# Optimization experiments

Measured on AMD Instinct MI355X. Metric: run time of the kernel, lower is better.

Reference implementation:

```python
import jax, jax.numpy as jnp
import numpy as np

ROUTES = 1152
CAPS = 10
IN_CH = 8
OUT_CH = 16
BATCH = 256
NUM_ITER = 3


def setup_inputs() -> dict:
    key = jax.random.key(0)
    kx, kw = jax.random.split(key)
    x = jax.random.normal(kx, (BATCH, ROUTES, IN_CH), dtype=jnp.float32)
    # W corresponds to nn.Parameter of shape [1, routes, caps, out, in]; leading 1 dropped.
    W = jax.random.normal(kw, (ROUTES, CAPS, OUT_CH, IN_CH), dtype=jnp.float32)
    return {"x": x, "W": W}


def _squash(s):
    # Faithful to source: sum of squares over the trailing singleton dim -> elementwise.
    sq = s * s
    return sq * s / ((1.0 + sq) * jnp.sqrt(sq))


def reference(x, W):
    # u_hat[b,r,c,o] = W[r,c,o,i] @ x[b,r,i]
    u_hat = jnp.einsum("rcoi,bri->brco", W, x)
    b_ij = jnp.zeros((ROUTES, CAPS), dtype=x.dtype)
    v = None
    for it in range(NUM_ITER):
        # legacy F.softmax on 4D [1,R,C,1] tensor -> softmax over dim=1 (routes)
        c_ij = jax.nn.softmax(b_ij, axis=0)  # [R, C]
        s_j = jnp.einsum("rc,brco->bco", c_ij, u_hat)  # [B, C, O]
        v = _squash(s_j)
        if it < NUM_ITER - 1:
            # a_ij[b,r,c] = <u_hat[b,r,c,:], v[b,c,:]>; b_ij += mean over batch
            a_ij = jnp.einsum("brco,bco->brc", u_hat, v)
            b_ij = b_ij + a_ij.mean(axis=0)
    # original returns v_j.squeeze(1) with shape [B, caps, out, 1]
    return v[..., None]
```

## Files before the change

### kernel.cpp

```cpp
#include <hip/hip_runtime.h>
#include <math.h>

namespace {

constexpr int B_ = 256;
constexpr int R_ = 1152;
constexpr int C_ = 10;
constexpr int O_ = 16;
constexpr int I_ = 8;
constexpr int CO_ = C_ * O_;
constexpr int WRI_ = C_ * O_ * I_;

constexpr int KS_  = 32;
constexpr int RC_  = R_ / KS_;

constexpr int NBA_   = 512;
constexpr int NBA2_  = 384;

constexpr int KSF_ = 16;
constexpr int RCF_ = R_ / KSF_;
constexpr int MBF_ = 16;

constexpr size_t XT_OFF    = 0;
constexpr size_t XT_N      = (size_t)R_ * B_ * I_;
constexpr size_t SA_OFF    = XT_OFF + XT_N;
constexpr size_t SAB_N     = (size_t)CO_ * B_;
constexpr size_t SB_OFF    = SA_OFF + SAB_N;
constexpr size_t BIJ_OFF   = SB_OFF + SAB_N;
constexpr size_t BIJ_N     = (size_t)C_ * R_;
constexpr size_t ZERO_N    = 2 * SAB_N + BIJ_N;
constexpr size_t FL_TOTAL  = BIJ_OFF + BIJ_N;

__device__ __forceinline__ float rcp_fast(float x) {
#if defined(__has_builtin)
#if __has_builtin(__builtin_amdgcn_rcpf)
    return __builtin_amdgcn_rcpf(x);
#else
    return 1.0f / x;
#endif
#else
    return 1.0f / x;
#endif
}

__device__ __forceinline__ float squashf(float s) {
    return s * fabsf(s) / (1.0f + s * s);
}

__device__ __forceinline__ float squash_fast(float s) {
    return s * fabsf(s) * rcp_fast(1.0f + s * s);
}

__global__ __launch_bounds__(256) void k_tr(const float* __restrict__ x,
                                            float* __restrict__ xT,
                                            float* __restrict__ zbase) {
    __shared__ float t[8][32][8];
    const int tid = threadIdx.x;
    {
        const int gi = blockIdx.x * 256 + tid;
        if (gi < (int)(ZERO_N / 4))
            ((float4*)zbase)[gi] = make_float4(0.f, 0.f, 0.f, 0.f);
    }
    const int r0 = (blockIdx.x % 36) * 32;
    const int b0 = (blockIdx.x / 36) * 8;
    {
        const int rl = tid & 31, bl = tid >> 5;
        const float4* p = (const float4*)(x + ((size_t)(b0 + bl) * R_ + (r0 + rl)) * I_);
        const float4 a0 = p[0], a1 = p[1];
        float* d = &t[bl][rl][0];
        *(float4*)d = a0;
        *(float4*)(d + 4) = a1;
    }
    __syncthreads();
    {
        const int f = tid & 7, rw = tid >> 3;
        const float* s8 = &t[f][rw][0];
        const float4 a0 = *(const float4*)s8, a1 = *(const float4*)(s8 + 4);
        float* d = xT + ((size_t)(r0 + rw) * B_ + (b0 + f)) * I_;
        *(float4*)d = a0;
        *(float4*)(d + 4) = a1;
    }
}

template <bool UNIFORM>
__global__ __launch_bounds__(256) void k_s8(const float* __restrict__ xT,
                                            const float* __restrict__ Wm,
                                            const float* __restrict__ bijT,
                                            float* __restrict__ s_dst) {
    __shared__ __align__(16) float wl[RC_ * 128];
    __shared__ float cwch[RC_];
    __shared__ float sred[8];

    const int tid   = threadIdx.x;
    const int lane  = tid & 63;
    const int bid   = blockIdx.x;
    const int c     = bid >> 6;
    const int chunk = bid & 63;
    const int ks    = chunk >> 1;
    const int bh    = chunk & 1;
    const int r0    = ks * RC_;

    if (!UNIFORM) {
        const float* bc = bijT + (size_t)c * R_;
        float bv[5];
        float m = -1e30f;
        #pragma unroll
        for (int k = 0; k < 5; ++k) {
            const int r = tid + 256 * k;
            bv[k] = (r < R_) ? bc[r] : -1e30f;
            m = fmaxf(m, bv[k]);
        }
        #pragma unroll
        for (int off = 32; off > 0; off >>= 1)
            m = fmaxf(m, __shfl_down(m, off, 64));
        if (lane == 0) sred[tid >> 6] = m;
        __syncthreads();
        const float bm = fmaxf(fmaxf(sred[0], sred[1]), fmaxf(sred[2], sred[3]));
        float se = 0.f;
        #pragma unroll
        for (int k = 0; k < 5; ++k)
            se += (bv[k] > -1e29f) ? expf(bv[k] - bm) : 0.f;
        #pragma unroll
        for (int off = 32; off > 0; off >>= 1)
            se += __shfl_down(se, off, 64);
        if (lane == 0) sred[4 + (tid >> 6)] = se;
        __syncthreads();
        const float inv = 1.0f / (sred[4] + sred[5] + sred[6] + sred[7]);
        if (tid < RC_) cwch[tid] = expf(bc[r0 + tid] - bm) * inv;
        __syncthreads();
    }

    {
        const float4* src = (const float4*)(Wm + ((size_t)r0 * C_ + c) * 128);
        float4* dst = (float4*)wl;
        #pragma unroll
        for (int k = 0; k < (RC_ * 32 + 255) / 256; ++k) {
            const int idx = tid + 256 * k;
            if (idx < RC_ * 32) {
                const int r = idx >> 5, q = idx & 31;
                float4 wv = src[(size_t)r * (C_ * 32) + q];
                const float cw = UNIFORM ? (1.0f / (float)R_) : cwch[r];
                wv.x *= cw; wv.y *= cw; wv.z *= cw; wv.w *= cw;
                dst[idx] = wv;
            }
        }
    }
    __syncthreads();

    const int o0 = (tid >> 6) * 4;
    const float* xbase = xT + ((size_t)r0 * B_ + bh * 128 + lane) * I_;

    float acc[4][2];
    #pragma unroll
    for (int oo = 0; oo < 4; ++oo) { acc[oo][0] = 0.f; acc[oo][1] = 0.f; }

    #pragma unroll 2
    for (int r = 0; r < RC_; ++r) {
        const float* xr = xbase + (size_t)r * B_ * I_;
        const float4 a00 = ((const float4*)xr)[0];
        const float4 a01 = ((const float4*)xr)[1];
        const float4 a10 = ((const float4*)(xr + 64 * I_))[0];
        const float4 a11 = ((const float4*)(xr + 64 * I_))[1];
        const float4* wp = (const float4*)&wl[r * 128 + o0 * 8];
        #pragma unroll
        for (int oo = 0; oo < 4; ++oo) {
            const float4 w0 = wp[oo * 2 + 0];
            const float4 w1 = wp[oo * 2 + 1];
            float a = acc[oo][0];
            a = fmaf(a00.x, w0.x, a);
            a = fmaf(a00.y, w0.y, a);
            a = fmaf(a00.z, w0.z, a);
            a = fmaf(a00.w, w0.w, a);
            a = fmaf(a01.x, w1.x, a);
            a = fmaf(a01.y, w1.y, a);
            a = fmaf(a01.z, w1.z, a);
            a = fmaf(a01.w, w1.w, a);
            acc[oo][0] = a;
            float b = acc[oo][1];
            b = fmaf(a10.x, w0.x, b);
            b = fmaf(a10.y, w0.y, b);
            b = fmaf(a10.z, w0.z, b);
            b = fmaf(a10.w, w0.w, b);
            b = fmaf(a11.x, w1.x, b);
            b = fmaf(a11.y, w1.y, b);
            b = fmaf(a11.z, w1.z, b);
            b = fmaf(a11.w, w1.w, b);
            acc[oo][1] = b;
        }
    }

    float* sp = s_dst + (size_t)(c * O_ + o0) * B_ + bh * 128 + lane;
    #pragma unroll
    for (int oo = 0; oo < 4; ++oo) {
        atomicAdd(sp + (size_t)oo * B_, acc[oo][0]);
        atomicAdd(sp + (size_t)oo * B_ + 64, acc[oo][1]);
    }
}

struct A8Sh {
    float4 xsw[3 * 512];
    float  part[3][320];
};

template <int NR>
__device__ __forceinline__ void a8_body(int r0, A8Sh& sh,
                                        const float* __restrict__ xT,
                                        const float* __restrict__ Wm,
                                        const float* __restrict__ s_read,
                                        float* __restrict__ bij_dst) {
    const int tid = threadIdx.x;

    {
        const float4* src = (const float4*)(xT + (size_t)r0 * B_ * I_);
        for (int k = tid; k < NR * 512; k += 320)
            sh.xsw[k ^ ((k >> 6) & 7)] = src[k];
    }
    __syncthreads();

    const int cq = tid % 40;
    const int bg = tid / 40;
    const int b0 = bg * 32;

    float acc[NR][4][8];
    #pragma unroll
    for (int rr = 0; rr < NR; ++rr)
        #pragma unroll
        for (int j = 0; j < 4; ++j)
            #pragma unroll
            for (int i = 0; i < 8; ++i) acc[rr][j][i] = 0.f;

    const float* vbase = s_read + (size_t)(4 * cq) * B_ + b0;

    #pragma unroll 2
    for (int bb = 0; bb < 32; bb += 4) {
        float va[4][4];
        #pragma unroll
        for (int j = 0; j < 4; ++j) {
            const float4 t = *(const float4*)(vbase + (size_t)j * B_ + bb);
            va[j][0] = squash_fast(t.x);
            va[j][1] = squash_fast(t.y);
            va[j][2] = squash_fast(t.z);
            va[j][3] = squash_fast(t.w);
        }
        #pragma unroll
        for (int j2 = 0; j2 < 4; ++j2) {
            const int eb = (b0 + bb + j2) * 2;
            #pragma unroll
            for (int rr = 0; rr < NR; ++rr) {
                const float4 x0 = sh.xsw[(rr * 512 + eb) ^ bg];
                const float4 x1 = sh.xsw[(rr * 512 + eb + 1) ^ bg];
                #pragma unroll
                for (int j = 0; j < 4; ++j) {
                    const float w = va[j][j2];
                    acc[rr][j][0] = fmaf(w, x0.x, acc[rr][j][0]);
                    acc[rr][j][1] = fmaf(w, x0.y, acc[rr][j][1]);
                    acc[rr][j][2] = fmaf(w, x0.z, acc[rr][j][2]);
                    acc[rr][j][3] = fmaf(w, x0.w, acc[rr][j][3]);
                    acc[rr][j][4] = fmaf(w, x1.x, acc[rr][j][4]);
                    acc[rr][j][5] = fmaf(w, x1.y, acc[rr][j][5]);
                    acc[rr][j][6] = fmaf(w, x1.z, acc[rr][j][6]);
                    acc[rr][j][7] = fmaf(w, x1.w, acc[rr][j][7]);
                }
            }
        }
    }

    #pragma unroll
    for (int rr = 0; rr < NR; ++rr) {
        const float* wp = Wm + (((size_t)(r0 + rr)) * CO_ + 4 * cq) * I_;
        float psum = 0.f;
        #pragma unroll
        for (int j = 0; j < 4; ++j) {
            const float4 w0 = *(const float4*)(wp + j * 8);
            const float4 w1 = *(const float4*)(wp + j * 8 + 4);
            float p = acc[rr][j][0] * w0.x;
            p = fmaf(acc[rr][j][1], w0.y, p);
            p = fmaf(acc[rr][j][2], w0.z, p);
            p = fmaf(acc[rr][j][3], w0.w, p);
            p = fmaf(acc[rr][j][4], w1.x, p);
            p = fmaf(acc[rr][j][5], w1.y, p);
            p = fmaf(acc[rr][j][6], w1.z, p);
            p = fmaf(acc[rr][j][7], w1.w, p);
            psum += p;
        }
        sh.part[rr][tid] = psum;
    }
    __syncthreads();

    if (tid < NR * C_) {
        const int r = tid / C_, c2 = tid % C_;
        float s = 0.f;
        #pragma unroll
        for (int g2 = 0; g2 < 8; ++g2)
            #pragma unroll
            for (int q = 0; q < 4; ++q)
                s += sh.part[r][g2 * 40 + c2 * 4 + q];
        bij_dst[(size_t)c2 * R_ + (r0 + r)] += s * (1.0f / (float)B_);
    }
}

__global__ __launch_bounds__(320) void k_a8(const float* __restrict__ xT,
                                            const float* __restrict__ Wm,
                                            const float* __restrict__ s_read,
                                            float* __restrict__ s_zero,
                                            float* __restrict__ bijT) {
    __shared__ A8Sh sh;
    const int bid = blockIdx.x;
    if (s_zero != nullptr && bid < 40 && threadIdx.x < 256) {
        ((float4*)s_zero)[bid * 256 + threadIdx.x] =
            make_float4(0.f, 0.f, 0.f, 0.f);
    }
    if (bid < NBA2_) {
        a8_body<2>(bid * 2, sh, xT, Wm, s_read, bijT);
    } else {
        a8_body<3>(NBA2_ * 2 + (bid - NBA2_) * 3, sh, xT, Wm, s_read, bijT);
    }
}

__global__ __launch_bounds__(256) void k_sqout(const float* __restrict__ s,
                                               float* __restrict__ out) {
    const int co = blockIdx.x;
    const int b  = threadIdx.x;
    out[(size_t)b * CO_ + co] = squash_fast(s[(size_t)co * B_ + b]);
}

template <bool UNIFORM>
__global__ __launch_bounds__(256) void k_s_f(const float* __restrict__ x,
                                             const float* __restrict__ Wm,
                                             const float* __restrict__ cij,
                                             float* __restrict__ s_out) {
    const int o  = threadIdx.x & 15;
    const int tb = threadIdx.x >> 4;
    const int b  = blockIdx.z * MBF_ + tb;
    const int c  = blockIdx.y;
    const int r0 = blockIdx.x * RCF_;

    const float* xp = x + ((size_t)b * R_ + r0) * I_;
    const float* wp = Wm + (((size_t)r0 * C_ + c) * O_ + o) * I_;
    const float* cp = cij + (size_t)r0 * C_ + c;

    float acc = 0.f;
    #pragma unroll 4
    for (int r = 0; r < RCF_; ++r) {
        const float4 xv0 = *(const float4*)(xp);
        const float4 xv1 = *(const float4*)(xp + 4);
        const float4 wv0 = *(const float4*)(wp);
        const float4 wv1 = *(const float4*)(wp + 4);
        const float p0 = fmaf(xv0.y, wv0.y, xv0.x * wv0.x);
        const float p1 = fmaf(xv0.w, wv0.w, xv0.z * wv0.z);
        const float p2 = fmaf(xv1.y, wv1.y, xv1.x * wv1.x);
        const float p3 = fmaf(xv1.w, wv1.w, xv1.z * wv1.z);
        const float cw = UNIFORM ? (1.0f / (float)R_) : cp[0];
        acc = fmaf(cw, (p0 + p1) + (p2 + p3), acc);
        xp += I_;
        wp += WRI_;
        cp += C_;
    }
    atomicAdd(&s_out[((size_t)b * C_ + c) * O_ + o], acc);
}

__global__ __launch_bounds__(256) void k_a_f(const float* __restrict__ x,
                                             const float* __restrict__ Wm,
                                             const float* __restrict__ s_in,
                                             float* __restrict__ amean) {
    __shared__ __align__(16) float wlds[2 * WRI_];
    __shared__ float red[4][2 * C_];

    const int tid = threadIdx.x;
    const int r0  = blockIdx.x * 2;

    const float* wsrc = Wm + (size_t)r0 * WRI_;
    #pragma unroll
    for (int k = 0; k < 2 * WRI_ / 256; ++k)
        wlds[tid + 256 * k] = wsrc[tid + 256 * k];
    __syncthreads();

    const int b    = tid;
    const int lane = tid & 63;
    const int wv   = tid >> 6;

    float xv[2][I_];
    const float4* xp4 = (const float4*)(x + ((size_t)b * R_ + r0) * I_);
    #pragma unroll
    for (int rr = 0; rr < 2; ++rr) {
        const float4 a0 = xp4[rr * 2 + 0];
        const float4 a1 = xp4[rr * 2 + 1];
        xv[rr][0] = a0.x; xv[rr][1] = a0.y; xv[rr][2] = a0.z; xv[rr][3] = a0.w;
        xv[rr][4] = a1.x; xv[rr][5] = a1.y; xv[rr][6] = a1.z; xv[rr][7] = a1.w;
    }

    #pragma unroll 1
    for (int c = 0; c < C_; ++c) {
        const float4* sp4 = (const float4*)(s_in + ((size_t)b * C_ + c) * O_);
        float v[O_];
        #pragma unroll
        for (int q = 0; q < 4; ++q) {
            const float4 sv = sp4[q];
            v[q * 4 + 0] = squashf(sv.x);
            v[q * 4 + 1] = squashf(sv.y);
            v[q * 4 + 2] = squashf(sv.z);
            v[q * 4 + 3] = squashf(sv.w);
        }
        #pragma unroll 1
        for (int rr = 0; rr < 2; ++rr) {
            const float4* wl4 = (const float4*)&wlds[(rr * C_ + c) * O_ * I_];
            float a = 0.f;
            #pragma unroll
            for (int o = 0; o < O_; ++o) {
                const float4 w0 = wl4[o * 2 + 0];
                const float4 w1 = wl4[o * 2 + 1];
                float u = xv[rr][0] * w0.x;
                u = fmaf(xv[rr][1], w0.y, u);
                u = fmaf(xv[rr][2], w0.z, u);
                u = fmaf(xv[rr][3], w0.w, u);
                u = fmaf(xv[rr][4], w1.x, u);
                u = fmaf(xv[rr][5], w1.y, u);
                u = fmaf(xv[rr][6], w1.z, u);
                u = fmaf(xv[rr][7], w1.w, u);
                a = fmaf(u, v[o], a);
            }
            #pragma unroll
            for (int off = 32; off > 0; off >>= 1)
                a += __shfl_down(a, off, 64);
            if (lane == 0) red[wv][rr * C_ + c] = a;
        }
    }

    __syncthreads();
    if (tid < 2 * C_) {
        const float t = red[0][tid] + red[1][tid] + red[2][tid] + red[3][tid];
        const int rr = tid / C_;
        const int c  = tid % C_;
        amean[(size_t)(r0 + rr) * C_ + c] = t * (1.0f / (float)B_);
    }
}

__global__ __launch_bounds__(256) void k_soft(const float* __restrict__ amean,
                                              float* __restrict__ bij,
                                              float* __restrict__ cij) {
    const int c   = blockIdx.x;
    const int tid = threadIdx.x;
    __shared__ float sred[4];

    float vals[5];
    float m = -1e30f;
    #pragma unroll
    for (int k = 0; k < 5; ++k) {
        const int r = tid + 256 * k;
        if (r < R_) {
            const size_t idx = (size_t)r * C_ + c;
            const float vv = bij[idx] + amean[idx];
            bij[idx] = vv;
            vals[k] = vv;
            m = fmaxf(m, vv);
        } else {
            vals[k] = -1e30f;
        }
    }
    #pragma unroll
    for (int off = 32; off > 0; off >>= 1)
        m = fmaxf(m, __shfl_down(m, off, 64));
    if ((tid & 63) == 0) sred[tid >> 6] = m;
    __syncthreads();
    const float bm = fmaxf(fmaxf(sred[0], sred[1]), fmaxf(sred[2], sred[3]));
    __syncthreads();

    float se = 0.f;
    #pragma unroll
    for (int k = 0; k < 5; ++k)
        se += (vals[k] > -1e29f) ? expf(vals[k] - bm) : 0.f;
    #pragma unroll
    for (int off = 32; off > 0; off >>= 1)
        se += __shfl_down(se, off, 64);
    if ((tid & 63) == 0) sred[tid >> 6] = se;
    __syncthreads();
    const float inv = 1.0f / (sred[0] + sred[1] + sred[2] + sred[3]);

    #pragma unroll
    for (int k = 0; k < 5; ++k) {
        const int r = tid + 256 * k;
        if (r < R_) cij[(size_t)r * C_ + c] = expf(vals[k] - bm) * inv;
    }
}

__global__ __launch_bounds__(256) void k_squash(float* __restrict__ s) {
    const int idx = blockIdx.x * 256 + threadIdx.x;
    if (idx < B_ * CO_) s[idx] = squashf(s[idx]);
}

}

extern "C" void kernel_launch(void* const* d_in, const int* in_sizes, int n_in,
                              void* d_out, int out_size, void* d_ws, size_t ws_size,
                              hipStream_t stream) {
    const float* x  = (const float*)d_in[0];
    const float* Wm = (const float*)d_in[1];
    float* out = (float*)d_out;
    float* ws  = (float*)d_ws;

    const size_t need = FL_TOTAL * sizeof(float);

    if (ws_size >= need) {
        float* xT   = ws + XT_OFF;
        float* sA   = ws + SA_OFF;
        float* sB   = ws + SB_OFF;
        float* bijT = ws + BIJ_OFF;

        k_tr<<<1152, 256, 0, stream>>>(x, xT, sA );

        k_s8<true><<<C_ * 64, 256, 0, stream>>>(xT, Wm, bijT, sA);
        k_a8<<<NBA_, 320, 0, stream>>>(xT, Wm, sA, nullptr, bijT);

        k_s8<false><<<C_ * 64, 256, 0, stream>>>(xT, Wm, bijT, sB);
        k_a8<<<NBA_, 320, 0, stream>>>(xT, Wm, sB, sA , bijT);

        k_s8<false><<<C_ * 64, 256, 0, stream>>>(xT, Wm, bijT, sA);
        k_sqout<<<CO_, 256, 0, stream>>>(sA, out);
    } else {
        float* s_buf = ws;
        float* cij   = ws + 40960;
        float* bij   = cij + R_ * C_;
        float* amean = bij + R_ * C_;

        const dim3 gsf(KSF_, C_, B_ / MBF_);

        hipMemsetAsync(bij, 0, R_ * C_ * sizeof(float), stream);

        hipMemsetAsync(s_buf, 0, B_ * CO_ * sizeof(float), stream);
        k_s_f<true><<<gsf, 256, 0, stream>>>(x, Wm, cij, s_buf);
        k_a_f<<<R_ / 2, 256, 0, stream>>>(x, Wm, s_buf, amean);
        k_soft<<<C_, 256, 0, stream>>>(amean, bij, cij);

        hipMemsetAsync(s_buf, 0, B_ * CO_ * sizeof(float), stream);
        k_s_f<false><<<gsf, 256, 0, stream>>>(x, Wm, cij, s_buf);
        k_a_f<<<R_ / 2, 256, 0, stream>>>(x, Wm, s_buf, amean);
        k_soft<<<C_, 256, 0, stream>>>(amean, bij, cij);

        hipMemsetAsync(out, 0, B_ * CO_ * sizeof(float), stream);
        k_s_f<false><<<gsf, 256, 0, stream>>>(x, Wm, cij, out);
        k_squash<<<(B_ * CO_ + 255) / 256, 256, 0, stream>>>(out);
    }
}
```

Baseline: 195.4 us.

## Split routing kernels across batch halves and double route-chunk count

The s-kernel now splits routes into 64 chunks instead of 32, doubling its grid. The agreement kernel is replaced by k_a9, which handles two routes per block for only half the batch, so there are twice as many blocks, each with less shared memory. Per-route b_ij updates now combine the two batch halves with atomicAdd instead of a plain accumulate. The aim is more parallelism and occupancy on the many-CU GPU, at the cost of more atomics on s and b_ij and smaller per-block work.

Result: slower. 202.0 us (+3.4%).

```diff
diff --git a/kernel.cpp b/kernel.cpp
--- a/kernel.cpp
+++ b/kernel.cpp
@@ -11,11 +11,11 @@
 constexpr int CO_ = C_ * O_;
 constexpr int WRI_ = C_ * O_ * I_;
 
-constexpr int KS_  = 32;
+constexpr int KS_  = 64;
 constexpr int RC_  = R_ / KS_;
 
-constexpr int NBA_   = 512;
-constexpr int NBA2_  = 384;
+constexpr int NRP_ = 576;
+constexpr int NBA_ = NRP_ * 2;
 
 constexpr int KSF_ = 16;
 constexpr int RCF_ = R_ / KSF_;
@@ -94,8 +94,8 @@
     const int tid   = threadIdx.x;
     const int lane  = tid & 63;
     const int bid   = blockIdx.x;
-    const int c     = bid >> 6;
-    const int chunk = bid & 63;
+    const int c     = bid >> 7;
+    const int chunk = bid & 127;
     const int ks    = chunk >> 1;
     const int bh    = chunk & 1;
     const int r0    = ks * RC_;
@@ -197,42 +197,52 @@
     }
 }
 
-struct A8Sh {
-    float4 xsw[3 * 512];
-    float  part[3][320];
+struct A9Sh {
+    float4 xsw[2 * 256];
+    float  part[2][320];
 };
 
-template <int NR>
-__device__ __forceinline__ void a8_body(int r0, A8Sh& sh,
-                                        const float* __restrict__ xT,
-                                        const float* __restrict__ Wm,
-                                        const float* __restrict__ s_read,
-                                        float* __restrict__ bij_dst) {
+__global__ __launch_bounds__(320) void k_a9(const float* __restrict__ xT,
+                                            const float* __restrict__ Wm,
+                                            const float* __restrict__ s_read,
+                                            float* __restrict__ s_zero,
+                                            float* __restrict__ bijT) {
+    __shared__ A9Sh sh;
     const int tid = threadIdx.x;
+    const int bid = blockIdx.x;
+    const int bh  = (bid >= NRP_) ? 1 : 0;
+    const int rp  = bid - bh * NRP_;
+    const int r0  = rp * 2;
+
+    if (s_zero != nullptr && bid < 40 && tid < 256) {
+        ((float4*)s_zero)[bid * 256 + tid] = make_float4(0.f, 0.f, 0.f, 0.f);
+    }
 
     {
         const float4* src = (const float4*)(xT + (size_t)r0 * B_ * I_);
-        for (int k = tid; k < NR * 512; k += 320)
-            sh.xsw[k ^ ((k >> 6) & 7)] = src[k];
+        for (int k = tid; k < 2 * 256; k += 320) {
+            const int rr = k >> 8, rem = k & 255;
+            sh.xsw[k ^ ((k >> 5) & 7)] = src[rr * 512 + bh * 256 + rem];
+        }
     }
     __syncthreads();
 
     const int cq = tid % 40;
     const int bg = tid / 40;
-    const int b0 = bg * 32;
-
-    float acc[NR][4][8];
-    #pragma unroll
-    for (int rr = 0; rr < NR; ++rr)
+    const int b0 = bg * 16;
+
+    float acc[2][4][8];
+    #pragma unroll
+    for (int rr = 0; rr < 2; ++rr)
         #pragma unroll
         for (int j = 0; j < 4; ++j)
             #pragma unroll
             for (int i = 0; i < 8; ++i) acc[rr][j][i] = 0.f;
 
-    const float* vbase = s_read + (size_t)(4 * cq) * B_ + b0;
+    const float* vbase = s_read + (size_t)(4 * cq) * B_ + bh * 128 + b0;
 
     #pragma unroll 2
-    for (int bb = 0; bb < 32; bb += 4) {
+    for (int bb = 0; bb < 16; bb += 4) {
         float va[4][4];
         #pragma unroll
         for (int j = 0; j < 4; ++j) {
@@ -246,9 +256,9 @@
         for (int j2 = 0; j2 < 4; ++j2) {
             const int eb = (b0 + bb + j2) * 2;
             #pragma unroll
-            for (int rr = 0; rr < NR; ++rr) {
-                const float4 x0 = sh.xsw[(rr * 512 + eb) ^ bg];
-                const float4 x1 = sh.xsw[(rr * 512 + eb + 1) ^ bg];
+            for (int rr = 0; rr < 2; ++rr) {
+                const float4 x0 = sh.xsw[(rr * 256 + eb) ^ bg];
+                const float4 x1 = sh.xsw[(rr * 256 + eb + 1) ^ bg];
                 #pragma unroll
                 for (int j = 0; j < 4; ++j) {
                     const float w = va[j][j2];
@@ -266,7 +276,7 @@
     }
 
     #pragma unroll
-    for (int rr = 0; rr < NR; ++rr) {
+    for (int rr = 0; rr < 2; ++rr) {
         const float* wp = Wm + (((size_t)(r0 + rr)) * CO_ + 4 * cq) * I_;
         float psum = 0.f;
         #pragma unroll
@@ -287,7 +297,7 @@
     }
     __syncthreads();
 
-    if (tid < NR * C_) {
+    if (tid < 2 * C_) {
         const int r = tid / C_, c2 = tid % C_;
         float s = 0.f;
         #pragma unroll
@@ -295,25 +305,7 @@
             #pragma unroll
             for (int q = 0; q < 4; ++q)
                 s += sh.part[r][g2 * 40 + c2 * 4 + q];
-        bij_dst[(size_t)c2 * R_ + (r0 + r)] += s * (1.0f / (float)B_);
-    }
-}
-
-__global__ __launch_bounds__(320) void k_a8(const float* __restrict__ xT,
-                                            const float* __restrict__ Wm,
-                                            const float* __restrict__ s_read,
-                                            float* __restrict__ s_zero,
-                                            float* __restrict__ bijT) {
-    __shared__ A8Sh sh;
-    const int bid = blockIdx.x;
-    if (s_zero != nullptr && bid < 40 && threadIdx.x < 256) {
-        ((float4*)s_zero)[bid * 256 + threadIdx.x] =
-            make_float4(0.f, 0.f, 0.f, 0.f);
-    }
-    if (bid < NBA2_) {
-        a8_body<2>(bid * 2, sh, xT, Wm, s_read, bijT);
-    } else {
-        a8_body<3>(NBA2_ * 2 + (bid - NBA2_) * 3, sh, xT, Wm, s_read, bijT);
+        atomicAdd(&bijT[(size_t)c2 * R_ + (r0 + r)], s * (1.0f / (float)B_));
     }
 }
 
@@ -508,13 +500,13 @@
 
         k_tr<<<1152, 256, 0, stream>>>(x, xT, sA );
 
-        k_s8<true><<<C_ * 64, 256, 0, stream>>>(xT, Wm, bijT, sA);
-        k_a8<<<NBA_, 320, 0, stream>>>(xT, Wm, sA, nullptr, bijT);
-
-        k_s8<false><<<C_ * 64, 256, 0, stream>>>(xT, Wm, bijT, sB);
-        k_a8<<<NBA_, 320, 0, stream>>>(xT, Wm, sB, sA , bijT);
-
-        k_s8<false><<<C_ * 64, 256, 0, stream>>>(xT, Wm, bijT, sA);
+        k_s8<true><<<C_ * 128, 256, 0, stream>>>(xT, Wm, bijT, sA);
+        k_a9<<<NBA_, 320, 0, stream>>>(xT, Wm, sA, nullptr, bijT);
+
+        k_s8<false><<<C_ * 128, 256, 0, stream>>>(xT, Wm, bijT, sB);
+        k_a9<<<NBA_, 320, 0, stream>>>(xT, Wm, sB, sA , bijT);
+
+        k_s8<false><<<C_ * 128, 256, 0, stream>>>(xT, Wm, bijT, sA);
         k_sqout<<<CO_, 256, 0, stream>>>(sA, out);
     } else {
         float* s_buf = ws;
```
